# Optimization experiments

Measured on AMD Instinct MI355X. Metric: run time of the kernel, lower is better.

## Reference

```python
import jax, jax.numpy as jnp
import numpy as np

DIM = 192
WIN = 7
HEADS = 6
SHIFT = 3
HID = 4 * DIM


def _ln(x, w, b, eps=1e-5):
    m = jnp.mean(x, axis=-1, keepdims=True)
    v = jnp.var(x, axis=-1, keepdims=True)
    return (x - m) * jax.lax.rsqrt(v + eps) * w + b


def setup_inputs() -> dict:
    key = jax.random.key(0)
    ks = jax.random.split(key, 8)
    B, C, H, W = 16, DIM, 56, 56
    s = lambda k, shape, fan: jax.random.normal(k, shape, jnp.float32) * (1.0 / np.sqrt(fan))
    return {
        "x": jax.random.normal(ks[0], (B, C, H, W), jnp.float32),
        "norm1_w": jnp.ones((C,), jnp.float32),
        "norm1_b": jnp.zeros((C,), jnp.float32),
        "qkv_w": s(ks[1], (3 * C, C), C),
        "qkv_b": jnp.zeros((3 * C,), jnp.float32),
        "proj_w": s(ks[2], (C, C), C),
        "proj_b": jnp.zeros((C,), jnp.float32),
        "norm2_w": jnp.ones((C,), jnp.float32),
        "norm2_b": jnp.zeros((C,), jnp.float32),
        "fc1_w": s(ks[3], (HID, C), C),
        "fc1_b": jnp.zeros((HID,), jnp.float32),
        "fc2_w": s(ks[4], (C, HID), HID),
        "fc2_b": jnp.zeros((C,), jnp.float32),
    }


def reference(x, norm1_w, norm1_b, qkv_w, qkv_b, proj_w, proj_b,
              norm2_w, norm2_b, fc1_w, fc1_b, fc2_w, fc2_b):
    B, C, H, W = x.shape
    shift = SHIFT if (H > WIN and W > WIN) else 0
    shortcut = x

    xl = jnp.transpose(x, (0, 2, 3, 1))            # B,H,W,C
    xl = _ln(xl, norm1_w, norm1_b)
    if shift > 0:
        xl = jnp.roll(xl, shift=(-shift, -shift), axis=(1, 2))
    nH, nW = H // WIN, W // WIN
    xw = xl.reshape(B, nH, WIN, nW, WIN, C)
    xw = jnp.transpose(xw, (0, 1, 3, 2, 4, 5)).reshape(-1, WIN * WIN, C)

    # window attention
    Bw, N, _ = xw.shape
    dh = C // HEADS
    qkv = jnp.einsum('bnc,oc->bno', xw, qkv_w) + qkv_b
    qkv = qkv.reshape(Bw, N, 3, HEADS, dh)
    q, k, v = qkv[:, :, 0], qkv[:, :, 1], qkv[:, :, 2]   # Bw,N,H,dh
    scale = dh ** -0.5
    attn = jnp.einsum('bnhd,bmhd->bhnm', q, k) * scale
    attn = jax.nn.softmax(attn, axis=-1)
    out = jnp.einsum('bhnm,bmhd->bnhd', attn, v).reshape(Bw, N, C)
    out = jnp.einsum('bnc,oc->bno', out, proj_w) + proj_b

    # window reverse -> B,H,W,C
    xl = out.reshape(B, nH, nW, WIN, WIN, C)
    xl = jnp.transpose(xl, (0, 1, 3, 2, 4, 5)).reshape(B, H, W, C)
    if shift > 0:
        xl = jnp.roll(xl, shift=(shift, shift), axis=(1, 2))

    # norm2 + MLP (note: original has NO attention residual)
    xl = _ln(xl, norm2_w, norm2_b)
    h = jnp.einsum('bhwc,oc->bhwo', xl, fc1_w) + fc1_b
    h = jax.nn.gelu(h, approximate=False)
    h = jnp.einsum('bhwo,co->bhwc', h, fc2_w) + fc2_b
    return jnp.transpose(h, (0, 3, 1, 2)) + shortcut
```

## Files before the change

### kernel.cpp

```cpp
#include <hip/hip_runtime.h>
#include <hip/hip_bf16.h>

typedef __bf16 bf16_t;
typedef __bf16 bf16x4 __attribute__((ext_vector_type(4)));
typedef __bf16 bf16x8 __attribute__((ext_vector_type(8)));
typedef float f32x4 __attribute__((ext_vector_type(4)));

#define MFMA16(a, b, c) __builtin_amdgcn_mfma_f32_16x16x32_bf16((a), (b), (c), 0, 0, 0)

__device__ __forceinline__ void gl16(const bf16_t* g, void* l) {
    __builtin_amdgcn_global_load_lds(
        (const __attribute__((address_space(1))) void*)g,
        (__attribute__((address_space(3))) void*)l, 16, 0, 0);
}

__device__ __forceinline__ float gelu_t(float u) {
    float t2 = fminf(u * (1.5957691216057308f + 0.07135481627f * u * u), 60.f);
    float e = __expf(t2);
    return u * e / (e + 1.f);
}


__global__ __launch_bounds__(256) void k_cvt(const float* __restrict__ qkvw,
                                             const float* __restrict__ projw,
                                             const float* __restrict__ fc1w,
                                             const float* __restrict__ fc2w,
                                             bf16_t* __restrict__ dst)
{
    int i = blockIdx.x * 256 + threadIdx.x;
    if (i >= 442368) return;
    float v;
    if (i < 110592)      v = qkvw[i];
    else if (i < 147456) v = projw[i - 110592];
    else if (i < 294912) v = fc1w[i - 147456];
    else                 v = fc2w[i - 294912];
    dst[i] = (bf16_t)v;
}

__global__ __launch_bounds__(1024) void k_ln1(const float* __restrict__ x,
                                              const float* __restrict__ gam,
                                              const float* __restrict__ bet,
                                              bf16_t* __restrict__ xw)
{
    __shared__ float tile[56][193];
    __shared__ bf16_t obuf[56 * 192];
    const int bh = blockIdx.x;
    const int b = bh / 56, h = bh % 56;
    const int tid = threadIdx.x;

    {
        const int g = tid >> 4, u = tid & 15;
        const float* xb = x + (long)b * 602112 + (long)h * 56;
        if (u < 14) {
            #pragma unroll
            for (int k = 0; k < 3; ++k) {
                const int c = g + 64 * k;
                float4 v = *(const float4*)(xb + (long)c * 3136 + u * 4);
                tile[u * 4 + 0][c] = v.x;
                tile[u * 4 + 1][c] = v.y;
                tile[u * 4 + 2][c] = v.z;
                tile[u * 4 + 3][c] = v.w;
            }
        }
    }
    __syncthreads();

    const int wave = tid >> 6, lane = tid & 63;
    const float g0 = gam[lane], g1 = gam[lane + 64], g2 = gam[lane + 128];
    const float b0 = bet[lane], b1 = bet[lane + 64], b2 = bet[lane + 128];
    for (int wp = wave; wp < 56; wp += 16) {
        float v0 = tile[wp][lane], v1 = tile[wp][lane + 64], v2 = tile[wp][lane + 128];
        float s = v0 + v1 + v2;
        float sq = v0 * v0 + v1 * v1 + v2 * v2;
        #pragma unroll
        for (int d = 1; d < 64; d <<= 1) { s += __shfl_xor(s, d); sq += __shfl_xor(sq, d); }
        float mean = s * (1.f / 192.f);
        float var  = sq * (1.f / 192.f) - mean * mean;
        float rs = rsqrtf(var + 1e-5f);
        const int wr = (wp + 53) % 56;
        bf16_t* o = obuf + wr * 192;
        o[lane]       = (bf16_t)((v0 - mean) * rs * g0 + b0);
        o[lane + 64]  = (bf16_t)((v1 - mean) * rs * g1 + b1);
        o[lane + 128] = (bf16_t)((v2 - mean) * rs * g2 + b2);
    }
    __syncthreads();

    const int hr = (h + 53) % 56;
    const int nh = hr / 7, ii = hr % 7;
    const long rband = ((long)b * 64 + (long)nh * 8) * 49 + (long)ii * 7;
    const int4* src = (const int4*)obuf;
    for (int q = tid; q < 1344; q += 1024) {
        const int g = q / 168, u = q % 168;
        const int jj = u / 24, ci = u % 24;
        const long r = rband + (long)g * 49 + jj;
        ((int4*)xw)[r * 24 + ci] = src[(g * 7 + jj) * 24 + ci];
    }
}

template<int EPI, int N, int K>
__global__ __launch_bounds__(256) void k_gemm192(const bf16_t* __restrict__ A,
                                                 const bf16_t* __restrict__ W,
                                                 const float* __restrict__ bias,
                                                 bf16_t* __restrict__ outp)
{
    constexpr int NT = K / 64;
    __shared__ bf16_t As[128 * 64];
    __shared__ bf16_t Bs[192 * 64];
    const int tid = threadIdx.x;
    const int wv = tid >> 6, ln = tid & 63;
    const int lrow = ln & 15, lkg = ln >> 4;
    const int r7 = lrow & 7;
    const int wm = (wv >> 1) * 64, wn = (wv & 1) * 96;
    const long m0 = (long)blockIdx.x * 128;
    const int n0 = blockIdx.y * 192;

    f32x4 acc[4][6];
    #pragma unroll
    for (int mi = 0; mi < 4; ++mi)
        #pragma unroll
        for (int ni = 0; ni < 6; ++ni)
            #pragma unroll
            for (int rg = 0; rg < 4; ++rg) acc[mi][ni][rg] = 0.f;

    for (int t = 0; t < NT; ++t) {
        #pragma unroll
        for (int i = 0; i < 4; ++i) {
            const int off = ((wv * 4 + i) << 10) + ln * 16;
            const int row = off >> 7;
            const int c16 = ((off >> 4) & 7) ^ (row & 7);
            gl16(A + (m0 + row) * K + t * 64 + (c16 << 3),
                 (char*)As + ((wv * 4 + i) << 10));
        }
        #pragma unroll
        for (int i = 0; i < 6; ++i) {
            const int off = ((wv * 6 + i) << 10) + ln * 16;
            const int row = off >> 7;
            const int c16 = ((off >> 4) & 7) ^ (row & 7);
            gl16(W + (long)(n0 + row) * K + t * 64 + (c16 << 3),
                 (char*)Bs + ((wv * 6 + i) << 10));
        }
        __syncthreads();
        #pragma unroll
        for (int kk = 0; kk < 2; ++kk) {
            const int kb = (((kk << 2) | lkg) ^ r7) << 4;
            bf16x8 af[4], bfr[6];
            #pragma unroll
            for (int mi = 0; mi < 4; ++mi)
                af[mi] = *(const bf16x8*)((const char*)As
                           + (wm + mi * 16 + lrow) * 128 + kb);
            #pragma unroll
            for (int ni = 0; ni < 6; ++ni)
                bfr[ni] = *(const bf16x8*)((const char*)Bs
                           + (wn + ni * 16 + lrow) * 128 + kb);
            #pragma unroll
            for (int mi = 0; mi < 4; ++mi)
                #pragma unroll
                for (int ni = 0; ni < 6; ++ni)
                    acc[mi][ni] = MFMA16(bfr[ni], af[mi], acc[mi][ni]);
        }
        __syncthreads();
    }

    #pragma unroll
    for (int mi = 0; mi < 4; ++mi) {
        const long m = m0 + wm + mi * 16 + lrow;
        #pragma unroll
        for (int ni = 0; ni < 6; ++ni) {
            const int nb = n0 + wn + ni * 16 + lkg * 4;
            const float4 bv = *(const float4*)(bias + nb);
            float v[4] = { acc[mi][ni][0] + bv.x, acc[mi][ni][1] + bv.y,
                           acc[mi][ni][2] + bv.z, acc[mi][ni][3] + bv.w };
            bf16x4 o;
            #pragma unroll
            for (int rg = 0; rg < 4; ++rg) {
                float u = v[rg];
                if (EPI == 2) u = gelu_t(u);
                o[rg] = (bf16_t)u;
            }
            *(bf16x4*)(outp + m * N + nb) = o;
        }
    }
}

template<int EPI, int N, int K>
__global__ __launch_bounds__(256) void k_gemm(const bf16_t* __restrict__ A,
                                              const bf16_t* __restrict__ W,
                                              const float* __restrict__ bias,
                                              bf16_t* __restrict__ outp)
{
    __shared__ bf16_t As[128 * 64];
    __shared__ bf16_t Bs[64 * 64];
    const int tid = threadIdx.x;
    const int wv = tid >> 6, ln = tid & 63;
    const int lrow = ln & 15, lkg = ln >> 4;
    const int r7 = lrow & 7;
    const int wm = (wv >> 1) * 64, wn = (wv & 1) * 32;
    const long m0 = (long)blockIdx.x * 128;
    const int n0 = blockIdx.y * 64;

    f32x4 acc[4][2];
    #pragma unroll
    for (int mi = 0; mi < 4; ++mi)
        #pragma unroll
        for (int ni = 0; ni < 2; ++ni)
            #pragma unroll
            for (int rg = 0; rg < 4; ++rg) acc[mi][ni][rg] = 0.f;

    for (int t = 0; t < K / 64; ++t) {
        #pragma unroll
        for (int i = 0; i < 4; ++i) {
            const int off = ((wv * 4 + i) << 10) + ln * 16;
            const int row = off >> 7;
            const int c16 = ((off >> 4) & 7) ^ (row & 7);
            gl16(A + (m0 + row) * K + t * 64 + (c16 << 3),
                 (char*)As + ((wv * 4 + i) << 10));
        }
        #pragma unroll
        for (int i = 0; i < 2; ++i) {
            const int off = ((wv * 2 + i) << 10) + ln * 16;
            const int row = off >> 7;
            const int c16 = ((off >> 4) & 7) ^ (row & 7);
            gl16(W + (long)(n0 + row) * K + t * 64 + (c16 << 3),
                 (char*)Bs + ((wv * 2 + i) << 10));
        }
        __syncthreads();
        #pragma unroll
        for (int kk = 0; kk < 2; ++kk) {
            const int kb = (((kk << 2) | lkg) ^ r7) << 4;
            bf16x8 af[4], bfr[2];
            #pragma unroll
            for (int mi = 0; mi < 4; ++mi)
                af[mi] = *(const bf16x8*)((const char*)As
                           + (wm + mi * 16 + lrow) * 128 + kb);
            #pragma unroll
            for (int ni = 0; ni < 2; ++ni)
                bfr[ni] = *(const bf16x8*)((const char*)Bs
                           + (wn + ni * 16 + lrow) * 128 + kb);
            #pragma unroll
            for (int mi = 0; mi < 4; ++mi)
                #pragma unroll
                for (int ni = 0; ni < 2; ++ni)
                    acc[mi][ni] = MFMA16(bfr[ni], af[mi], acc[mi][ni]);
        }
        __syncthreads();
    }

    #pragma unroll
    for (int mi = 0; mi < 4; ++mi) {
        const long m = m0 + wm + mi * 16 + lrow;
        #pragma unroll
        for (int ni = 0; ni < 2; ++ni) {
            const int nb = n0 + wn + ni * 16 + lkg * 4;
            const float4 bv = *(const float4*)(bias + nb);
            float v[4] = { acc[mi][ni][0] + bv.x, acc[mi][ni][1] + bv.y,
                           acc[mi][ni][2] + bv.z, acc[mi][ni][3] + bv.w };
            bf16x4 o;
            #pragma unroll
            for (int rg = 0; rg < 4; ++rg) {
                float u = v[rg];
                if (EPI == 2) u = gelu_t(u);
                o[rg] = (bf16_t)u;
            }
            *(bf16x4*)(outp + m * N + nb) = o;
        }
    }
}

__global__ __launch_bounds__(256) void k_proj_ln(const bf16_t* __restrict__ A,
                                                 const bf16_t* __restrict__ W,
                                                 const float* __restrict__ bias,
                                                 const float* __restrict__ gam,
                                                 const float* __restrict__ bet,
                                                 bf16_t* __restrict__ out)
{
    __shared__ bf16_t As[128][72];
    __shared__ bf16_t Bs[192][72];
    const int tid = threadIdx.x;
    const int wave = tid >> 6, lane = tid & 63;
    const int lrow = lane & 15, lkg = lane >> 4;
    const int wm = wave * 32;
    const long m0 = (long)blockIdx.x * 128;

    f32x4 acc[2][12];
    #pragma unroll
    for (int mi = 0; mi < 2; ++mi)
        #pragma unroll
        for (int ni = 0; ni < 12; ++ni)
            #pragma unroll
            for (int rg = 0; rg < 4; ++rg) acc[mi][ni][rg] = 0.f;

    for (int k0 = 0; k0 < 192; k0 += 64) {
        #pragma unroll
        for (int it = 0; it < 4; ++it) {
            int e = (tid + it * 256) * 8;
            int r = e >> 6, c = e & 63;
            *(int4*)(&As[r][c]) = *(const int4*)(A + (m0 + r) * 192 + (k0 + c));
        }
        #pragma unroll
        for (int it = 0; it < 6; ++it) {
            int e = (tid + it * 256) * 8;
            int r = e >> 6, c = e & 63;
            *(int4*)(&Bs[r][c]) = *(const int4*)(W + (long)r * 192 + (k0 + c));
        }
        __syncthreads();
        #pragma unroll
        for (int kk = 0; kk < 64; kk += 32) {
            bf16x8 af[2];
            #pragma unroll
            for (int mi = 0; mi < 2; ++mi)
                af[mi] = *(const bf16x8*)(&As[wm + mi * 16 + lrow][kk + lkg * 8]);
            #pragma unroll
            for (int ni = 0; ni < 12; ++ni) {
                bf16x8 bfr = *(const bf16x8*)(&Bs[ni * 16 + lrow][kk + lkg * 8]);
                acc[0][ni] = MFMA16(af[0], bfr, acc[0][ni]);
                acc[1][ni] = MFMA16(af[1], bfr, acc[1][ni]);
            }
        }
        __syncthreads();
    }

    float bv[12];
    #pragma unroll
    for (int ni = 0; ni < 12; ++ni) bv[ni] = bias[ni * 16 + lrow];

    #pragma unroll
    for (int mi = 0; mi < 2; ++mi) {
        #pragma unroll
        for (int rg = 0; rg < 4; ++rg) {
            float val[12];
            float s = 0.f, sq = 0.f;
            #pragma unroll
            for (int ni = 0; ni < 12; ++ni) {
                val[ni] = acc[mi][ni][rg] + bv[ni];
                s += val[ni];
                sq += val[ni] * val[ni];
            }
            #pragma unroll
            for (int d = 1; d < 16; d <<= 1) {
                s += __shfl_xor(s, d);
                sq += __shfl_xor(sq, d);
            }
            float mean = s * (1.f / 192.f);
            float var  = sq * (1.f / 192.f) - mean * mean;
            float rs = rsqrtf(var + 1e-5f);
            const long row = m0 + wm + mi * 16 + lkg * 4 + rg;
            bf16_t* orow = out + row * 192;
            #pragma unroll
            for (int ni = 0; ni < 12; ++ni) {
                const int col = ni * 16 + lrow;
                orow[col] = (bf16_t)((val[ni] - mean) * rs * gam[col] + bet[col]);
            }
        }
    }
}

__global__ __launch_bounds__(64) void k_attn(const bf16_t* __restrict__ qkv,
                                             bf16_t* __restrict__ aout)
{
    __shared__ bf16_t Pl[64][72];
    __shared__ bf16_t Vt[32][72];
    const int win = blockIdx.x, head = blockIdx.y;
    const int lane = threadIdx.x;
    const int lrow = lane & 15, lkg = lane >> 4;
    const bf16_t* base = qkv + (long)win * 28224 + head * 32;

    {
        const int m = lane;
        const int mc = (m < 49) ? m : 48;
        const int4* vr = (const int4*)(base + (long)mc * 576 + 384);
        #pragma unroll
        for (int c4 = 0; c4 < 4; ++c4) {
            int4 vv = vr[c4];
            if (m >= 49) vv = make_int4(0, 0, 0, 0);
            const bf16_t* pe = (const bf16_t*)&vv;
            #pragma unroll
            for (int e = 0; e < 8; ++e) Vt[c4 * 8 + e][m] = pe[e];
        }
    }

    bf16x8 z8;
    #pragma unroll
    for (int e = 0; e < 8; ++e) z8[e] = (bf16_t)0.f;
    bf16x8 qf[4], kf[4];
    #pragma unroll
    for (int t = 0; t < 4; ++t) {
        const int n = t * 16 + lrow;
        const int nc = (n < 49) ? n : 48;
        bf16x8 qv = *(const bf16x8*)(base + (long)nc * 576 + lkg * 8);
        bf16x8 kv = *(const bf16x8*)(base + (long)nc * 576 + 192 + lkg * 8);
        qf[t] = (n < 49) ? qv : z8;
        kf[t] = (n < 49) ? kv : z8;
    }
    f32x4 zf; zf[0] = zf[1] = zf[2] = zf[3] = 0.f;
    f32x4 S[4][4];
    #pragma unroll
    for (int mi = 0; mi < 4; ++mi)
        #pragma unroll
        for (int mj = 0; mj < 4; ++mj)
            S[mi][mj] = MFMA16(qf[mi], kf[mj], zf);

    const float scl = 0.17677669529663687f;
    #pragma unroll
    for (int mi = 0; mi < 4; ++mi) {
        #pragma unroll
        for (int rg = 0; rg < 4; ++rg) {
            float v0 = S[mi][0][rg] * scl;
            float v1 = S[mi][1][rg] * scl;
            float v2 = S[mi][2][rg] * scl;
            float v3 = (lrow == 0) ? S[mi][3][rg] * scl : -1e30f;
            float mx = fmaxf(fmaxf(v0, v1), fmaxf(v2, v3));
            #pragma unroll
            for (int d = 1; d < 16; d <<= 1) mx = fmaxf(mx, __shfl_xor(mx, d));
            float e0 = expf(v0 - mx), e1 = expf(v1 - mx), e2 = expf(v2 - mx);
            float e3 = (lrow == 0) ? expf(v3 - mx) : 0.f;
            float sm = e0 + e1 + e2 + e3;
            #pragma unroll
            for (int d = 1; d < 16; d <<= 1) sm += __shfl_xor(sm, d);
            float is = 1.f / sm;
            const int row = mi * 16 + lkg * 4 + rg;
            Pl[row][lrow]      = (bf16_t)(e0 * is);
            Pl[row][16 + lrow] = (bf16_t)(e1 * is);
            Pl[row][32 + lrow] = (bf16_t)(e2 * is);
            Pl[row][48 + lrow] = (bf16_t)(e3 * is);
        }
    }
    __syncthreads();

    f32x4 o[4][2];
    #pragma unroll
    for (int ni = 0; ni < 4; ++ni)
        #pragma unroll
        for (int di = 0; di < 2; ++di)
            #pragma unroll
            for (int rg = 0; rg < 4; ++rg) o[ni][di][rg] = 0.f;
    #pragma unroll
    for (int m0 = 0; m0 < 64; m0 += 32) {
        bf16x8 pf[4], vf[2];
        #pragma unroll
        for (int ni = 0; ni < 4; ++ni)
            pf[ni] = *(const bf16x8*)(&Pl[ni * 16 + lrow][m0 + lkg * 8]);
        #pragma unroll
        for (int di = 0; di < 2; ++di)
            vf[di] = *(const bf16x8*)(&Vt[di * 16 + lrow][m0 + lkg * 8]);
        #pragma unroll
        for (int ni = 0; ni < 4; ++ni)
            #pragma unroll
            for (int di = 0; di < 2; ++di)
                o[ni][di] = MFMA16(pf[ni], vf[di], o[ni][di]);
    }
    #pragma unroll
    for (int ni = 0; ni < 4; ++ni) {
        #pragma unroll
        for (int rg = 0; rg < 4; ++rg) {
            const int n = ni * 16 + lkg * 4 + rg;
            if (n < 49) {
                bf16_t* orow = aout + ((long)win * 49 + n) * 192 + head * 32;
                orow[lrow]      = (bf16_t)o[ni][0][rg];
                orow[16 + lrow] = (bf16_t)o[ni][1][rg];
            }
        }
    }
}

__global__ __launch_bounds__(1024) void k_final(const bf16_t* __restrict__ fb,
                                                const float* __restrict__ x,
                                                float* __restrict__ out)
{
    __shared__ float tile[56][199];
    const int bh = blockIdx.x;
    const int b = bh / 56, hq = bh % 56;
    const int tid = threadIdx.x;
    const int hr = (hq + 53) % 56;
    const int nh = hr / 7, ii = hr % 7;
    const long rband = ((long)b * 64 + (long)nh * 8) * 49 + (long)ii * 7;

    for (int q = tid; q < 1344; q += 1024) {
        const int g = q / 168, rem = q % 168;
        const int jj = rem / 24, ci = rem % 24;
        const long rr = rband + (long)g * 49 + jj;
        bf16x8 v = *(const bf16x8*)(fb + rr * 192 + ci * 8);
        const int wq = (g * 7 + jj + 3) % 56;
        #pragma unroll
        for (int e = 0; e < 8; ++e) tile[wq][ci * 8 + e] = (float)v[e];
    }
    __syncthreads();

    const int g = tid >> 4, u = tid & 15;
    if (u < 14) {
        #pragma unroll
        for (int k = 0; k < 3; ++k) {
            const int c = g + 64 * k;
            const long base = ((long)b * 192 + c) * 3136 + (long)hq * 56 + u * 4;
            float4 xv = *(const float4*)(x + base);
            float4 ov;
            ov.x = tile[u * 4 + 0][c] + xv.x;
            ov.y = tile[u * 4 + 1][c] + xv.y;
            ov.z = tile[u * 4 + 2][c] + xv.z;
            ov.w = tile[u * 4 + 3][c] + xv.w;
            *(float4*)(out + base) = ov;
        }
    }
}

extern "C" void kernel_launch(void* const* d_in, const int* in_sizes, int n_in,
                              void* d_out, int out_size, void* d_ws, size_t ws_size,
                              hipStream_t stream)
{
    const float* x     = (const float*)d_in[0];
    const float* n1w   = (const float*)d_in[1];
    const float* n1b   = (const float*)d_in[2];
    const float* qkvw  = (const float*)d_in[3];
    const float* qkvb  = (const float*)d_in[4];
    const float* projw = (const float*)d_in[5];
    const float* projb = (const float*)d_in[6];
    const float* n2w   = (const float*)d_in[7];
    const float* n2b   = (const float*)d_in[8];
    const float* fc1w  = (const float*)d_in[9];
    const float* fc1b  = (const float*)d_in[10];
    const float* fc2w  = (const float*)d_in[11];
    const float* fc2b  = (const float*)d_in[12];

    char* ws = (char*)d_ws;
    bf16_t* wqkv  = (bf16_t*)(ws);
    bf16_t* wproj = (bf16_t*)(ws + 221184);
    bf16_t* wfc1  = (bf16_t*)(ws + 294912);
    bf16_t* wfc2  = (bf16_t*)(ws + 589824);
    bf16_t* Xb    = (bf16_t*)(ws + 884736);
    bf16_t* QKV   = (bf16_t*)(ws + 20152320);
    bf16_t* Hb    = (bf16_t*)(ws + 77955072);
    bf16_t* H2    = (bf16_t*)(ws + 155025408);
    bf16_t* X2    = (bf16_t*)(ws + 174292992);

    k_cvt<<<1728, 256, 0, stream>>>(qkvw, projw, fc1w, fc2w, wqkv);
    k_ln1<<<896, 1024, 0, stream>>>(x, n1w, n1b, Xb);
    k_gemm192<0, 576, 192><<<dim3(392, 3), 256, 0, stream>>>(Xb, wqkv, qkvb, QKV);
    k_attn<<<dim3(1024, 6), 64, 0, stream>>>(QKV, Xb);
    k_proj_ln<<<392, 256, 0, stream>>>(Xb, wproj, projb, n2w, n2b, X2);
    k_gemm192<2, 768, 192><<<dim3(392, 4), 256, 0, stream>>>(X2, wfc1, fc1b, Hb);
    k_gemm<0, 192, 768><<<dim3(392, 3), 256, 0, stream>>>(Hb, wfc2, fc2b, H2);
    k_final<<<896, 1024, 0, stream>>>(H2, x, (float*)d_out);
}
```

Before: 244.8 us.

## Use smaller single-stage 64x64 tiles for K=192 GEMMs and proj_ln

```diff
diff --git a/kernel.cpp b/kernel.cpp
--- a/kernel.cpp
+++ b/kernel.cpp
@@ -97,75 +97,73 @@
     }
 }
 
-template<int EPI, int N, int K>
-__global__ __launch_bounds__(256) void k_gemm192(const bf16_t* __restrict__ A,
+template<int EPI, int N>
+__global__ __launch_bounds__(256) void k_gemm_1s(const bf16_t* __restrict__ A,
                                                  const bf16_t* __restrict__ W,
                                                  const float* __restrict__ bias,
                                                  bf16_t* __restrict__ outp)
 {
-    constexpr int NT = K / 64;
-    __shared__ bf16_t As[128 * 64];
-    __shared__ bf16_t Bs[192 * 64];
+    __shared__ bf16_t As[64 * 192];
+    __shared__ bf16_t Bs[64 * 192];
     const int tid = threadIdx.x;
     const int wv = tid >> 6, ln = tid & 63;
     const int lrow = ln & 15, lkg = ln >> 4;
     const int r7 = lrow & 7;
-    const int wm = (wv >> 1) * 64, wn = (wv & 1) * 96;
-    const long m0 = (long)blockIdx.x * 128;
-    const int n0 = blockIdx.y * 192;
-
-    f32x4 acc[4][6];
-    #pragma unroll
-    for (int mi = 0; mi < 4; ++mi)
-        #pragma unroll
-        for (int ni = 0; ni < 6; ++ni)
+    const int wm = (wv >> 1) * 32, wn = (wv & 1) * 32;
+    const long m0 = (long)blockIdx.x * 64;
+    const int n0 = blockIdx.y * 64;
+
+    #pragma unroll
+    for (int i = 0; i < 6; ++i) {
+        const int off = ((wv * 6 + i) << 10) + ln * 16;
+        const int row = off / 384;
+        const int slot = (off % 384) >> 4;
+        const int col = ((slot & 24) | ((slot & 7) ^ (row & 7))) << 3;
+        gl16(A + (m0 + row) * 192 + col, (char*)As + ((wv * 6 + i) << 10));
+    }
+    #pragma unroll
+    for (int i = 0; i < 6; ++i) {
+        const int off = ((wv * 6 + i) << 10) + ln * 16;
+        const int row = off / 384;
+        const int slot = (off % 384) >> 4;
+        const int col = ((slot & 24) | ((slot & 7) ^ (row & 7))) << 3;
+        gl16(W + (long)(n0 + row) * 192 + col, (char*)Bs + ((wv * 6 + i) << 10));
+    }
+    __syncthreads();
+
+    f32x4 acc[2][2];
+    #pragma unroll
+    for (int mi = 0; mi < 2; ++mi)
+        #pragma unroll
+        for (int ni = 0; ni < 2; ++ni)
             #pragma unroll
             for (int rg = 0; rg < 4; ++rg) acc[mi][ni][rg] = 0.f;
 
-    for (int t = 0; t < NT; ++t) {
-        #pragma unroll
-        for (int i = 0; i < 4; ++i) {
-            const int off = ((wv * 4 + i) << 10) + ln * 16;
-            const int row = off >> 7;
-            const int c16 = ((off >> 4) & 7) ^ (row & 7);
-            gl16(A + (m0 + row) * K + t * 64 + (c16 << 3),
-                 (char*)As + ((wv * 4 + i) << 10));
-        }
-        #pragma unroll
-        for (int i = 0; i < 6; ++i) {
-            const int off = ((wv * 6 + i) << 10) + ln * 16;
-            const int row = off >> 7;
-            const int c16 = ((off >> 4) & 7) ^ (row & 7);
-            gl16(W + (long)(n0 + row) * K + t * 64 + (c16 << 3),
-                 (char*)Bs + ((wv * 6 + i) << 10));
-        }
-        __syncthreads();
-        #pragma unroll
-        for (int kk = 0; kk < 2; ++kk) {
-            const int kb = (((kk << 2) | lkg) ^ r7) << 4;
-            bf16x8 af[4], bfr[6];
-            #pragma unroll
-            for (int mi = 0; mi < 4; ++mi)
-                af[mi] = *(const bf16x8*)((const char*)As
-                           + (wm + mi * 16 + lrow) * 128 + kb);
-            #pragma unroll
-            for (int ni = 0; ni < 6; ++ni)
-                bfr[ni] = *(const bf16x8*)((const char*)Bs
-                           + (wn + ni * 16 + lrow) * 128 + kb);
-            #pragma unroll
-            for (int mi = 0; mi < 4; ++mi)
-                #pragma unroll
-                for (int ni = 0; ni < 6; ++ni)
-                    acc[mi][ni] = MFMA16(bfr[ni], af[mi], acc[mi][ni]);
-        }
-        __syncthreads();
-    }
-
-    #pragma unroll
-    for (int mi = 0; mi < 4; ++mi) {
+    #pragma unroll
+    for (int kk = 0; kk < 6; ++kk) {
+        const int s = kk * 4 + lkg;
+        const int kb = ((s & 24) | ((s & 7) ^ r7)) << 4;
+        bf16x8 af[2], bfr[2];
+        #pragma unroll
+        for (int mi = 0; mi < 2; ++mi)
+            af[mi] = *(const bf16x8*)((const char*)As
+                       + (wm + mi * 16 + lrow) * 384 + kb);
+        #pragma unroll
+        for (int ni = 0; ni < 2; ++ni)
+            bfr[ni] = *(const bf16x8*)((const char*)Bs
+                       + (wn + ni * 16 + lrow) * 384 + kb);
+        #pragma unroll
+        for (int mi = 0; mi < 2; ++mi)
+            #pragma unroll
+            for (int ni = 0; ni < 2; ++ni)
+                acc[mi][ni] = MFMA16(bfr[ni], af[mi], acc[mi][ni]);
+    }
+
+    #pragma unroll
+    for (int mi = 0; mi < 2; ++mi) {
         const long m = m0 + wm + mi * 16 + lrow;
         #pragma unroll
-        for (int ni = 0; ni < 6; ++ni) {
+        for (int ni = 0; ni < 2; ++ni) {
             const int nb = n0 + wn + ni * 16 + lkg * 4;
             const float4 bv = *(const float4*)(bias + nb);
             float v[4] = { acc[mi][ni][0] + bv.x, acc[mi][ni][1] + bv.y,
@@ -273,25 +271,23 @@
                                                  const float* __restrict__ bet,
                                                  bf16_t* __restrict__ out)
 {
-    __shared__ bf16_t As[128][72];
+    __shared__ bf16_t As[64][72];
     __shared__ bf16_t Bs[192][72];
     const int tid = threadIdx.x;
     const int wave = tid >> 6, lane = tid & 63;
     const int lrow = lane & 15, lkg = lane >> 4;
-    const int wm = wave * 32;
-    const long m0 = (long)blockIdx.x * 128;
-
-    f32x4 acc[2][12];
-    #pragma unroll
-    for (int mi = 0; mi < 2; ++mi)
-        #pragma unroll
-        for (int ni = 0; ni < 12; ++ni)
-            #pragma unroll
-            for (int rg = 0; rg < 4; ++rg) acc[mi][ni][rg] = 0.f;
+    const int wm = wave * 16;
+    const long m0 = (long)blockIdx.x * 64;
+
+    f32x4 acc[12];
+    #pragma unroll
+    for (int ni = 0; ni < 12; ++ni)
+        #pragma unroll
+        for (int rg = 0; rg < 4; ++rg) acc[ni][rg] = 0.f;
 
     for (int k0 = 0; k0 < 192; k0 += 64) {
         #pragma unroll
-        for (int it = 0; it < 4; ++it) {
+        for (int it = 0; it < 2; ++it) {
             int e = (tid + it * 256) * 8;
             int r = e >> 6, c = e & 63;
             *(int4*)(&As[r][c]) = *(const int4*)(A + (m0 + r) * 192 + (k0 + c));
@@ -305,15 +301,11 @@
         __syncthreads();
         #pragma unroll
         for (int kk = 0; kk < 64; kk += 32) {
-            bf16x8 af[2];
-            #pragma unroll
-            for (int mi = 0; mi < 2; ++mi)
-                af[mi] = *(const bf16x8*)(&As[wm + mi * 16 + lrow][kk + lkg * 8]);
+            bf16x8 af = *(const bf16x8*)(&As[wm + lrow][kk + lkg * 8]);
             #pragma unroll
             for (int ni = 0; ni < 12; ++ni) {
                 bf16x8 bfr = *(const bf16x8*)(&Bs[ni * 16 + lrow][kk + lkg * 8]);
-                acc[0][ni] = MFMA16(af[0], bfr, acc[0][ni]);
-                acc[1][ni] = MFMA16(af[1], bfr, acc[1][ni]);
+                acc[ni] = MFMA16(af, bfr, acc[ni]);
             }
         }
         __syncthreads();
@@ -324,32 +316,29 @@
     for (int ni = 0; ni < 12; ++ni) bv[ni] = bias[ni * 16 + lrow];
 
     #pragma unroll
-    for (int mi = 0; mi < 2; ++mi) {
-        #pragma unroll
-        for (int rg = 0; rg < 4; ++rg) {
-            float val[12];
-            float s = 0.f, sq = 0.f;
-            #pragma unroll
-            for (int ni = 0; ni < 12; ++ni) {
-                val[ni] = acc[mi][ni][rg] + bv[ni];
-                s += val[ni];
-                sq += val[ni] * val[ni];
-            }
-            #pragma unroll
-            for (int d = 1; d < 16; d <<= 1) {
-                s += __shfl_xor(s, d);
-                sq += __shfl_xor(sq, d);
-            }
-            float mean = s * (1.f / 192.f);
-            float var  = sq * (1.f / 192.f) - mean * mean;
-            float rs = rsqrtf(var + 1e-5f);
-            const long row = m0 + wm + mi * 16 + lkg * 4 + rg;
-            bf16_t* orow = out + row * 192;
-            #pragma unroll
-            for (int ni = 0; ni < 12; ++ni) {
-                const int col = ni * 16 + lrow;
-                orow[col] = (bf16_t)((val[ni] - mean) * rs * gam[col] + bet[col]);
-            }
+    for (int rg = 0; rg < 4; ++rg) {
+        float val[12];
+        float s = 0.f, sq = 0.f;
+        #pragma unroll
+        for (int ni = 0; ni < 12; ++ni) {
+            val[ni] = acc[ni][rg] + bv[ni];
+            s += val[ni];
+            sq += val[ni] * val[ni];
+        }
+        #pragma unroll
+        for (int d = 1; d < 16; d <<= 1) {
+            s += __shfl_xor(s, d);
+            sq += __shfl_xor(sq, d);
+        }
+        float mean = s * (1.f / 192.f);
+        float var  = sq * (1.f / 192.f) - mean * mean;
+        float rs = rsqrtf(var + 1e-5f);
+        const long row = m0 + wm + lkg * 4 + rg;
+        bf16_t* orow = out + row * 192;
+        #pragma unroll
+        for (int ni = 0; ni < 12; ++ni) {
+            const int col = ni * 16 + lrow;
+            orow[col] = (bf16_t)((val[ni] - mean) * rs * gam[col] + bet[col]);
         }
     }
 }
@@ -533,10 +522,10 @@
 
     k_cvt<<<1728, 256, 0, stream>>>(qkvw, projw, fc1w, fc2w, wqkv);
     k_ln1<<<896, 1024, 0, stream>>>(x, n1w, n1b, Xb);
-    k_gemm192<0, 576, 192><<<dim3(392, 3), 256, 0, stream>>>(Xb, wqkv, qkvb, QKV);
+    k_gemm_1s<0, 576><<<dim3(784, 9), 256, 0, stream>>>(Xb, wqkv, qkvb, QKV);
     k_attn<<<dim3(1024, 6), 64, 0, stream>>>(QKV, Xb);
-    k_proj_ln<<<392, 256, 0, stream>>>(Xb, wproj, projb, n2w, n2b, X2);
-    k_gemm192<2, 768, 192><<<dim3(392, 4), 256, 0, stream>>>(X2, wfc1, fc1b, Hb);
+    k_proj_ln<<<784, 256, 0, stream>>>(Xb, wproj, projb, n2w, n2b, X2);
+    k_gemm_1s<2, 768><<<dim3(784, 12), 256, 0, stream>>>(X2, wfc1, fc1b, Hb);
     k_gemm<0, 192, 768><<<dim3(392, 3), 256, 0, stream>>>(Hb, wfc2, fc2b, H2);
     k_final<<<896, 1024, 0, stream>>>(H2, x, (float*)d_out);
 }
```

Measured after the change: 210.1 us. 1.17x faster.
